# Optimization experiments

Measured on AMD Instinct MI355X. Metric: run time of the kernel, lower is better.

Reference implementation:

```python
import jax, jax.numpy as jnp
import numpy as np

B, LQ, LK, D = 8, 2048, 2048, 128
NEG = -100000.0


def setup_inputs() -> dict:
    key = jax.random.key(0)
    kq, kk, kv, km = jax.random.split(key, 4)
    q = jax.random.normal(kq, (B, LQ, D), dtype=jnp.float32)
    k = jax.random.normal(kk, (B, LK, D), dtype=jnp.float32)
    v = jax.random.normal(kv, (B, LK, D), dtype=jnp.float32)
    mask = jax.random.randint(km, (B, LQ, LK), 0, 2, dtype=jnp.int32)
    return {"q": q, "k": k, "v": v, "mask": mask}


def reference(q, k, v, mask):
    # atten_score = q @ k^T / sqrt(d)   [B, Lq, Lk]
    scores = jnp.einsum("bqd,bkd->bqk", q, k) / jnp.sqrt(jnp.float32(q.shape[-1]))
    # mask_mod == 2: additive mask, masked positions pushed to large negative
    scores = scores + mask.astype(jnp.float32) * NEG
    # sigmoid instead of softmax (no normalization across keys)
    attn = jax.nn.sigmoid(scores)
    return jnp.einsum("bqk,bkd->bqd", attn, v)
```

## Files before the change

### kernel.cpp

```cpp
#include <hip/hip_runtime.h>
#include <hip/hip_bf16.h>

#define B_   8
#define LQ_  2048
#define LK_  2048
#define D_   128
#define QBLK 64
#define THREADS 512
#define NITER 16
#define NEGL2E (-0.12755004910797864f)

typedef __attribute__((ext_vector_type(8))) __bf16 bf16x8;
typedef __attribute__((ext_vector_type(4))) float  f32x4;
typedef __attribute__((ext_vector_type(4))) float  fx4;
typedef __attribute__((ext_vector_type(4))) int    i32x4;

__global__ __launch_bounds__(256)
void kprep(const float* __restrict__ k, __bf16* __restrict__ kp)
{
    int id   = blockIdx.x * 256 + threadIdx.x;
    int lane = id & 63;
    int f    = id >> 6;
    int dblk = f & 3, kk = (f >> 2) & 127, b = f >> 9;
    const float* src = k + ((size_t)b * LK_ + kk * 16 + (lane & 15)) * D_
                         + dblk * 32 + (lane >> 4) * 8;
    fx4 f0 = *(const fx4*)src;
    fx4 f1 = *(const fx4*)(src + 4);
    bf16x8 w;
#pragma unroll
    for (int j = 0; j < 4; ++j) { w[j] = (__bf16)f0[j]; w[4 + j] = (__bf16)f1[j]; }
    *(bf16x8*)(kp + (size_t)f * 512 + lane * 8) = w;
}

__global__ __launch_bounds__(256)
void vprep(const float* __restrict__ v, __bf16* __restrict__ vp)
{
    int id   = blockIdx.x * 256 + threadIdx.x;
    int lane = id & 63;
    int f    = id >> 6;
    int nb = f & 7, ck = (f >> 3) & 63, b = f >> 9;
    int l15 = lane & 15, g = lane >> 4;
    bf16x8 w;
#pragma unroll
    for (int e = 0; e < 8; ++e) {
        int key = ck * 32 + (e >> 2) * 16 + g * 4 + (e & 3);
        w[e] = (__bf16)v[((size_t)b * LK_ + key) * D_ + nb * 16 + l15];
    }
    *(bf16x8*)(vp + (size_t)f * 512 + lane * 8) = w;
}

__global__ __launch_bounds__(THREADS, 2)
void sigattn_main(const float* __restrict__ q, const int* __restrict__ mask,
                  const __bf16* __restrict__ Kp, const __bf16* __restrict__ Vp,
                  float* __restrict__ out)
{
    __shared__ __align__(16) char smem[64 * 132 * 4];
    unsigned char* bitsbuf = (unsigned char*)smem;

    const int tid  = threadIdx.x;
    const int lane = tid & 63;
    const int l15  = lane & 15;
    const int g    = lane >> 4;
    const int wid  = tid >> 6;
    const int qg   = wid & 1;
    const int kq   = wid >> 1;
    const int qbase = qg * 32;

    const int bid = blockIdx.x;
    const int b   = bid & 7;
    const int q0  = (bid >> 3) * QBLK;

    const float*  qb = q    + ((size_t)b * LQ_ + q0) * D_;
    const int*    mb = mask + ((size_t)b * LQ_ + q0) * LK_;
    const __bf16* kp = Kp + (size_t)b * 262144;
    const __bf16* vp = Vp + (size_t)b * 262144;
    float*        ob = out  + ((size_t)b * LQ_ + q0) * D_;

    bf16x8 qfrag[2][4];
#pragma unroll
    for (int qq = 0; qq < 2; ++qq) {
        const float* qrow = qb + (size_t)(qbase + qq * 16 + l15) * D_;
#pragma unroll
        for (int dblk = 0; dblk < 4; ++dblk) {
            fx4 f0 = *(const fx4*)(qrow + dblk * 32 + g * 8);
            fx4 f1 = *(const fx4*)(qrow + dblk * 32 + g * 8 + 4);
            bf16x8 w;
#pragma unroll
            for (int j = 0; j < 4; ++j) { w[j] = (__bf16)f0[j]; w[4 + j] = (__bf16)f1[j]; }
            qfrag[qq][dblk] = w;
        }
    }

    const int prow = wid * 8 + (lane >> 5);
    const int pk4  = lane & 31;
    const int* mrow = mb + (size_t)prow * LK_ + pk4 * 4;

    {
        i32x4 m4[4];
#pragma unroll
        for (int j = 0; j < 4; ++j)
            m4[j] = __builtin_nontemporal_load((const i32x4*)(mrow + (size_t)(j * 2) * LK_));
#pragma unroll
        for (int j = 0; j < 4; ++j) {
            unsigned int nib = (m4[j][0] != 0 ? 1u : 0u) | (m4[j][1] != 0 ? 2u : 0u)
                             | (m4[j][2] != 0 ? 4u : 0u) | (m4[j][3] != 0 ? 8u : 0u);
            bitsbuf[(prow + j * 2) * 40 + pk4] = (unsigned char)nib;
        }
    }
    bf16x8 Kc[2][4];
#pragma unroll
    for (int ksl = 0; ksl < 2; ++ksl)
#pragma unroll
        for (int dblk = 0; dblk < 4; ++dblk)
            Kc[ksl][dblk] = *(const bf16x8*)(kp + (size_t)(((kq * 2 + ksl) * 4 + dblk)) * 512 + lane * 8);

    asm volatile("s_waitcnt lgkmcnt(0)\n\ts_barrier" ::: "memory");

    f32x4 oacc[2][8];
#pragma unroll
    for (int qq = 0; qq < 2; ++qq)
#pragma unroll
        for (int nb = 0; nb < 8; ++nb) oacc[qq][nb] = (f32x4){0.f, 0.f, 0.f, 0.f};

    for (int i = 0; i < NITER; ++i) {
        const bool more = (i + 1 < NITER);

        bf16x8 vfr[8];
#pragma unroll
        for (int nb = 0; nb < 8; ++nb)
            vfr[nb] = *(const bf16x8*)(vp + (size_t)(((i * 4 + kq) * 8 + nb)) * 512 + lane * 8);

        i32x4 m4[4];
        if (more) {
#pragma unroll
            for (int j = 0; j < 4; ++j)
                m4[j] = __builtin_nontemporal_load(
                    (const i32x4*)(mrow + (size_t)(i + 1) * 128 + (size_t)(j * 2) * LK_));
        }

        f32x4 sacc[2][2];
#pragma unroll
        for (int qq = 0; qq < 2; ++qq)
#pragma unroll
            for (int ksl = 0; ksl < 2; ++ksl) sacc[qq][ksl] = (f32x4){0.f, 0.f, 0.f, 0.f};
#pragma unroll
        for (int ksl = 0; ksl < 2; ++ksl)
#pragma unroll
            for (int dblk = 0; dblk < 4; ++dblk) {
                bf16x8 a = Kc[ksl][dblk];
#pragma unroll
                for (int qq = 0; qq < 2; ++qq)
                    sacc[qq][ksl] = __builtin_amdgcn_mfma_f32_16x16x32_bf16(a, qfrag[qq][dblk], sacc[qq][ksl], 0, 0, 0);
            }

        bf16x8 Kn[2][4];
        if (more) {
#pragma unroll
            for (int ksl = 0; ksl < 2; ++ksl)
#pragma unroll
                for (int dblk = 0; dblk < 4; ++dblk)
                    Kn[ksl][dblk] = *(const bf16x8*)(kp + (size_t)((((i + 1) * 8 + kq * 2 + ksl) * 4 + dblk)) * 512 + lane * 8);
        }

        bf16x8 pfrag[2];
#pragma unroll
        for (int qq = 0; qq < 2; ++qq) {
            const int rrow = (qbase + qq * 16 + l15) * 40;
            unsigned int b0 = bitsbuf[(i & 1) * 2560 + rrow + kq * 8 + g];
            unsigned int b1 = bitsbuf[(i & 1) * 2560 + rrow + kq * 8 + 4 + g];
#pragma unroll
            for (int ksl = 0; ksl < 2; ++ksl) {
                unsigned int bb = ksl ? b1 : b0;
#pragma unroll
                for (int r = 0; r < 4; ++r) {
                    float e = exp2f(sacc[qq][ksl][r] * NEGL2E);
                    float p = __builtin_amdgcn_rcpf(1.0f + e);
                    p = ((bb >> r) & 1u) ? 0.0f : p;
                    pfrag[qq][ksl * 4 + r] = (__bf16)p;
                }
            }
        }

#pragma unroll
        for (int nb = 0; nb < 8; ++nb)
#pragma unroll
            for (int qq = 0; qq < 2; ++qq)
                oacc[qq][nb] = __builtin_amdgcn_mfma_f32_16x16x32_bf16(pfrag[qq], vfr[nb], oacc[qq][nb], 0, 0, 0);

        if (more) {
#pragma unroll
            for (int j = 0; j < 4; ++j) {
                unsigned int nib = (m4[j][0] != 0 ? 1u : 0u) | (m4[j][1] != 0 ? 2u : 0u)
                                 | (m4[j][2] != 0 ? 4u : 0u) | (m4[j][3] != 0 ? 8u : 0u);
                bitsbuf[((i + 1) & 1) * 2560 + (prow + j * 2) * 40 + pk4] = (unsigned char)nib;
            }
        }

        asm volatile("s_waitcnt lgkmcnt(0)\n\ts_barrier" ::: "memory");

        if (more) {
#pragma unroll
            for (int ksl = 0; ksl < 2; ++ksl)
#pragma unroll
                for (int dblk = 0; dblk < 4; ++dblk)
                    Kc[ksl][dblk] = Kn[ksl][dblk];
        }
    }

    __syncthreads();
    float* red = (float*)smem;
    if (kq == 0) {
#pragma unroll
        for (int qq = 0; qq < 2; ++qq)
#pragma unroll
            for (int nb = 0; nb < 8; ++nb)
#pragma unroll
                for (int r = 0; r < 4; ++r)
                    red[(qbase + qq * 16 + 4 * g + r) * 132 + nb * 16 + l15] = oacc[qq][nb][r];
    }
    __syncthreads();
    if (kq == 1) {
#pragma unroll
        for (int qq = 0; qq < 2; ++qq)
#pragma unroll
            for (int nb = 0; nb < 8; ++nb)
#pragma unroll
                for (int r = 0; r < 4; ++r)
                    red[(qbase + qq * 16 + 4 * g + r) * 132 + nb * 16 + l15] += oacc[qq][nb][r];
    }
    __syncthreads();
    if (kq == 2) {
#pragma unroll
        for (int qq = 0; qq < 2; ++qq)
#pragma unroll
            for (int nb = 0; nb < 8; ++nb)
#pragma unroll
                for (int r = 0; r < 4; ++r)
                    red[(qbase + qq * 16 + 4 * g + r) * 132 + nb * 16 + l15] += oacc[qq][nb][r];
    }
    __syncthreads();
    if (kq == 3) {
#pragma unroll
        for (int qq = 0; qq < 2; ++qq)
#pragma unroll
            for (int nb = 0; nb < 8; ++nb)
#pragma unroll
                for (int r = 0; r < 4; ++r)
                    red[(qbase + qq * 16 + 4 * g + r) * 132 + nb * 16 + l15] += oacc[qq][nb][r];
    }
    __syncthreads();
#pragma unroll
    for (int i2 = 0; i2 < 4; ++i2) {
        int idx = tid + i2 * THREADS;
        int row = idx >> 5, c4 = idx & 31;
        fx4 val = *(const fx4*)(red + row * 132 + c4 * 4);
        __builtin_nontemporal_store(val, (fx4*)(ob + (size_t)row * D_ + c4 * 4));
    }
}

extern "C" void kernel_launch(void* const* d_in, const int* in_sizes, int n_in,
                              void* d_out, int out_size, void* d_ws, size_t ws_size,
                              hipStream_t stream) {
    const float* q    = (const float*)d_in[0];
    const float* k    = (const float*)d_in[1];
    const float* v    = (const float*)d_in[2];
    const int*   mask = (const int*)d_in[3];
    float*       out  = (float*)d_out;

    __bf16* Kp = (__bf16*)d_ws;
    __bf16* Vp = (__bf16*)d_ws + (size_t)2097152;

    kprep<<<dim3(1024), dim3(256), 0, stream>>>(k, Kp);
    vprep<<<dim3(1024), dim3(256), 0, stream>>>(v, Vp);
    sigattn_main<<<dim3(256), dim3(THREADS), 0, stream>>>(q, mask, Kp, Vp, out);
}
```

Measured before the change: 233.9 us.

## Pack mask to bits in a prep kernel and drop per-iteration LDS barriers

Adds a separate mprep kernel that packs the int32 mask into a bitmask (one byte per 8 keys) in workspace. The main kernel then loads packed bits straight from global memory into registers, removing the LDS bit buffer and the per-iteration barrier. It also merges the K and V prep kernels into one launch and unrolls the main loop by two. The mask is still read once in full, now in a separate pass that adds its own launch plus a write and re-read of the packed mask. In exchange the main loop loses its synchronisation and LDS traffic.

```diff
diff --git a/kernel.cpp b/kernel.cpp
--- a/kernel.cpp
+++ b/kernel.cpp
@@ -16,46 +16,63 @@
 typedef __attribute__((ext_vector_type(4))) int    i32x4;
 
 __global__ __launch_bounds__(256)
-void kprep(const float* __restrict__ k, __bf16* __restrict__ kp)
+void mprep(const int* __restrict__ mask, unsigned char* __restrict__ mp)
 {
-    int id   = blockIdx.x * 256 + threadIdx.x;
-    int lane = id & 63;
-    int f    = id >> 6;
-    int dblk = f & 3, kk = (f >> 2) & 127, b = f >> 9;
-    const float* src = k + ((size_t)b * LK_ + kk * 16 + (lane & 15)) * D_
-                         + dblk * 32 + (lane >> 4) * 8;
-    fx4 f0 = *(const fx4*)src;
-    fx4 f1 = *(const fx4*)(src + 4);
-    bf16x8 w;
-#pragma unroll
-    for (int j = 0; j < 4; ++j) { w[j] = (__bf16)f0[j]; w[4 + j] = (__bf16)f1[j]; }
-    *(bf16x8*)(kp + (size_t)f * 512 + lane * 8) = w;
+    size_t t = (size_t)blockIdx.x * 256 + threadIdx.x;
+    const int* src = mask + t * 8;
+    i32x4 a = *(const i32x4*)src;
+    i32x4 c = *(const i32x4*)(src + 4);
+    unsigned int v = 0;
+    v |= (a[0] != 0 ? 1u : 0u);
+    v |= (a[1] != 0 ? 2u : 0u);
+    v |= (a[2] != 0 ? 4u : 0u);
+    v |= (a[3] != 0 ? 8u : 0u);
+    v |= (c[0] != 0 ? 16u : 0u);
+    v |= (c[1] != 0 ? 32u : 0u);
+    v |= (c[2] != 0 ? 64u : 0u);
+    v |= (c[3] != 0 ? 128u : 0u);
+    mp[t] = (unsigned char)v;
 }
 
 __global__ __launch_bounds__(256)
-void vprep(const float* __restrict__ v, __bf16* __restrict__ vp)
+void kvprep(const float* __restrict__ k, const float* __restrict__ v,
+            __bf16* __restrict__ kp, __bf16* __restrict__ vp)
 {
-    int id   = blockIdx.x * 256 + threadIdx.x;
-    int lane = id & 63;
-    int f    = id >> 6;
-    int nb = f & 7, ck = (f >> 3) & 63, b = f >> 9;
-    int l15 = lane & 15, g = lane >> 4;
-    bf16x8 w;
-#pragma unroll
-    for (int e = 0; e < 8; ++e) {
-        int key = ck * 32 + (e >> 2) * 16 + g * 4 + (e & 3);
-        w[e] = (__bf16)v[((size_t)b * LK_ + key) * D_ + nb * 16 + l15];
-    }
-    *(bf16x8*)(vp + (size_t)f * 512 + lane * 8) = w;
+    int id = blockIdx.x * 256 + threadIdx.x;
+    if (id < 262144) {
+        int lane = id & 63;
+        int f    = id >> 6;
+        int dblk = f & 3, kk = (f >> 2) & 127, b = f >> 9;
+        const float* src = k + ((size_t)b * LK_ + kk * 16 + (lane & 15)) * D_
+                             + dblk * 32 + (lane >> 4) * 8;
+        fx4 f0 = *(const fx4*)src;
+        fx4 f1 = *(const fx4*)(src + 4);
+        bf16x8 w;
+#pragma unroll
+        for (int j = 0; j < 4; ++j) { w[j] = (__bf16)f0[j]; w[4 + j] = (__bf16)f1[j]; }
+        *(bf16x8*)(kp + (size_t)f * 512 + lane * 8) = w;
+    } else {
+        int id2  = id - 262144;
+        int lane = id2 & 63;
+        int f    = id2 >> 6;
+        int nb = f & 7, ck = (f >> 3) & 63, b = f >> 9;
+        int l15 = lane & 15, g = lane >> 4;
+        bf16x8 w;
+#pragma unroll
+        for (int e = 0; e < 8; ++e) {
+            int key = ck * 32 + (e >> 2) * 16 + g * 4 + (e & 3);
+            w[e] = (__bf16)v[((size_t)b * LK_ + key) * D_ + nb * 16 + l15];
+        }
+        *(bf16x8*)(vp + (size_t)f * 512 + lane * 8) = w;
+    }
 }
 
 __global__ __launch_bounds__(THREADS, 2)
-void sigattn_main(const float* __restrict__ q, const int* __restrict__ mask,
+void sigattn_main(const float* __restrict__ q, const unsigned char* __restrict__ mp,
                   const __bf16* __restrict__ Kp, const __bf16* __restrict__ Vp,
                   float* __restrict__ out)
 {
-    __shared__ __align__(16) char smem[64 * 132 * 4];
-    unsigned char* bitsbuf = (unsigned char*)smem;
+    __shared__ float red[64 * 132];
 
     const int tid  = threadIdx.x;
     const int lane = tid & 63;
@@ -70,11 +87,11 @@
     const int b   = bid & 7;
     const int q0  = (bid >> 3) * QBLK;
 
-    const float*  qb = q    + ((size_t)b * LQ_ + q0) * D_;
-    const int*    mb = mask + ((size_t)b * LQ_ + q0) * LK_;
-    const __bf16* kp = Kp + (size_t)b * 262144;
-    const __bf16* vp = Vp + (size_t)b * 262144;
-    float*        ob = out  + ((size_t)b * LQ_ + q0) * D_;
+    const float*         qb  = q  + ((size_t)b * LQ_ + q0) * D_;
+    const unsigned char* mpb = mp + ((size_t)b * LQ_ + q0) * 256;
+    const __bf16*        kp  = Kp + (size_t)b * 262144;
+    const __bf16*        vp  = Vp + (size_t)b * 262144;
+    float*               ob  = out + ((size_t)b * LQ_ + q0) * D_;
 
     bf16x8 qfrag[2][4];
 #pragma unroll
@@ -91,30 +108,20 @@
         }
     }
 
-    const int prow = wid * 8 + (lane >> 5);
-    const int pk4  = lane & 31;
-    const int* mrow = mb + (size_t)prow * LK_ + pk4 * 4;
-
-    {
-        i32x4 m4[4];
-#pragma unroll
-        for (int j = 0; j < 4; ++j)
-            m4[j] = __builtin_nontemporal_load((const i32x4*)(mrow + (size_t)(j * 2) * LK_));
-#pragma unroll
-        for (int j = 0; j < 4; ++j) {
-            unsigned int nib = (m4[j][0] != 0 ? 1u : 0u) | (m4[j][1] != 0 ? 2u : 0u)
-                             | (m4[j][2] != 0 ? 4u : 0u) | (m4[j][3] != 0 ? 8u : 0u);
-            bitsbuf[(prow + j * 2) * 40 + pk4] = (unsigned char)nib;
-        }
-    }
+    const unsigned char* maddr[2];
+#pragma unroll
+    for (int qq = 0; qq < 2; ++qq)
+        maddr[qq] = mpb + (size_t)(qbase + qq * 16 + l15) * 256 + kq * 4;
+
     bf16x8 Kc[2][4];
 #pragma unroll
     for (int ksl = 0; ksl < 2; ++ksl)
 #pragma unroll
         for (int dblk = 0; dblk < 4; ++dblk)
-            Kc[ksl][dblk] = *(const bf16x8*)(kp + (size_t)(((kq * 2 + ksl) * 4 + dblk)) * 512 + lane * 8);
-
-    asm volatile("s_waitcnt lgkmcnt(0)\n\ts_barrier" ::: "memory");
+            Kc[ksl][dblk] = *(const bf16x8*)(kp + (size_t)((kq * 2 + ksl) * 4 + dblk) * 512 + lane * 8);
+    unsigned int mc[2];
+#pragma unroll
+    for (int qq = 0; qq < 2; ++qq) mc[qq] = *(const unsigned int*)(maddr[qq]);
 
     f32x4 oacc[2][8];
 #pragma unroll
@@ -122,20 +129,26 @@
 #pragma unroll
         for (int nb = 0; nb < 8; ++nb) oacc[qq][nb] = (f32x4){0.f, 0.f, 0.f, 0.f};
 
+#pragma unroll 2
     for (int i = 0; i < NITER; ++i) {
         const bool more = (i + 1 < NITER);
 
         bf16x8 vfr[8];
 #pragma unroll
         for (int nb = 0; nb < 8; ++nb)
-            vfr[nb] = *(const bf16x8*)(vp + (size_t)(((i * 4 + kq) * 8 + nb)) * 512 + lane * 8);
-
-        i32x4 m4[4];
+            vfr[nb] = *(const bf16x8*)(vp + (size_t)((i * 4 + kq) * 8 + nb) * 512 + lane * 8);
+
+        bf16x8 Kn[2][4];
+        unsigned int mn[2];
         if (more) {
 #pragma unroll
-            for (int j = 0; j < 4; ++j)
-                m4[j] = __builtin_nontemporal_load(
-                    (const i32x4*)(mrow + (size_t)(i + 1) * 128 + (size_t)(j * 2) * LK_));
+            for (int ksl = 0; ksl < 2; ++ksl)
+#pragma unroll
+                for (int dblk = 0; dblk < 4; ++dblk)
+                    Kn[ksl][dblk] = *(const bf16x8*)(kp + (size_t)(((i + 1) * 8 + kq * 2 + ksl) * 4 + dblk) * 512 + lane * 8);
+#pragma unroll
+            for (int qq = 0; qq < 2; ++qq)
+                mn[qq] = *(const unsigned int*)(maddr[qq] + (i + 1) * 16);
         }
 
         f32x4 sacc[2][2];
@@ -153,24 +166,12 @@
                     sacc[qq][ksl] = __builtin_amdgcn_mfma_f32_16x16x32_bf16(a, qfrag[qq][dblk], sacc[qq][ksl], 0, 0, 0);
             }
 
-        bf16x8 Kn[2][4];
-        if (more) {
-#pragma unroll
-            for (int ksl = 0; ksl < 2; ++ksl)
-#pragma unroll
-                for (int dblk = 0; dblk < 4; ++dblk)
-                    Kn[ksl][dblk] = *(const bf16x8*)(kp + (size_t)((((i + 1) * 8 + kq * 2 + ksl) * 4 + dblk)) * 512 + lane * 8);
-        }
-
         bf16x8 pfrag[2];
 #pragma unroll
         for (int qq = 0; qq < 2; ++qq) {
-            const int rrow = (qbase + qq * 16 + l15) * 40;
-            unsigned int b0 = bitsbuf[(i & 1) * 2560 + rrow + kq * 8 + g];
-            unsigned int b1 = bitsbuf[(i & 1) * 2560 + rrow + kq * 8 + 4 + g];
 #pragma unroll
             for (int ksl = 0; ksl < 2; ++ksl) {
-                unsigned int bb = ksl ? b1 : b0;
+                const unsigned int bb = (mc[qq] >> (ksl * 16 + 4 * g)) & 0xFu;
 #pragma unroll
                 for (int r = 0; r < 4; ++r) {
                     float e = exp2f(sacc[qq][ksl][r] * NEGL2E);
@@ -189,26 +190,15 @@
 
         if (more) {
 #pragma unroll
-            for (int j = 0; j < 4; ++j) {
-                unsigned int nib = (m4[j][0] != 0 ? 1u : 0u) | (m4[j][1] != 0 ? 2u : 0u)
-                                 | (m4[j][2] != 0 ? 4u : 0u) | (m4[j][3] != 0 ? 8u : 0u);
-                bitsbuf[((i + 1) & 1) * 2560 + (prow + j * 2) * 40 + pk4] = (unsigned char)nib;
-            }
-        }
-
-        asm volatile("s_waitcnt lgkmcnt(0)\n\ts_barrier" ::: "memory");
-
-        if (more) {
-#pragma unroll
             for (int ksl = 0; ksl < 2; ++ksl)
 #pragma unroll
                 for (int dblk = 0; dblk < 4; ++dblk)
                     Kc[ksl][dblk] = Kn[ksl][dblk];
-        }
-    }
-
-    __syncthreads();
-    float* red = (float*)smem;
+            mc[0] = mn[0]; mc[1] = mn[1];
+        }
+    }
+
+    __syncthreads();
     if (kq == 0) {
 #pragma unroll
         for (int qq = 0; qq < 2; ++qq)
@@ -267,10 +257,11 @@
     const int*   mask = (const int*)d_in[3];
     float*       out  = (float*)d_out;
 
-    __bf16* Kp = (__bf16*)d_ws;
-    __bf16* Vp = (__bf16*)d_ws + (size_t)2097152;
-
-    kprep<<<dim3(1024), dim3(256), 0, stream>>>(k, Kp);
-    vprep<<<dim3(1024), dim3(256), 0, stream>>>(v, Vp);
-    sigattn_main<<<dim3(256), dim3(THREADS), 0, stream>>>(q, mask, Kp, Vp, out);
-}
+    __bf16*        Kp = (__bf16*)d_ws;
+    __bf16*        Vp = (__bf16*)d_ws + (size_t)2097152;
+    unsigned char* Mp = (unsigned char*)d_ws + (size_t)8388608;
+
+    mprep<<<dim3(16384), dim3(256), 0, stream>>>(mask, Mp);
+    kvprep<<<dim3(2048), dim3(256), 0, stream>>>(k, v, Kp, Vp);
+    sigattn_main<<<dim3(256), dim3(THREADS), 0, stream>>>(q, Mp, Kp, Vp, out);
+}
```

New measurement: 245.1 us. 1.05x slower.
